# Kernel optimization log

Measured on AMD Instinct MI355X. Metric: run time of the kernel, lower is better.

The kernel has to match this reference:

```python
import jax, jax.numpy as jnp
import numpy as np

SIGMA = 1.0

def setup_inputs() -> dict:
    key = jax.random.key(0)
    k1, k2 = jax.random.split(key)
    N, IN, OUT = 524288, 64, 128
    x = jax.random.normal(k1, (N, IN), dtype=jnp.float32)
    bin_centers = jax.random.normal(k2, (OUT, IN), dtype=jnp.float32)
    return {"x": x, "bin_centers": bin_centers}

def reference(x, bin_centers):
    # distances[n,o] = sum_i (x[n,i] - c[o,i])^2 = ||x_n||^2 - 2 x_n.c_o + ||c_o||^2
    x2 = jnp.sum(x * x, axis=1)[:, None]                # [N,1]
    c2 = jnp.sum(bin_centers * bin_centers, axis=1)[None, :]  # [1,O]
    xc = jnp.einsum('ni,oi->no', x, bin_centers)        # [N,O] GEMM
    distances = x2 - 2.0 * xc + c2                      # [N,O]
    rbf = jnp.exp(-distances / (2.0 * SIGMA ** 2))      # [N,O]
    # histogram[o,i] = sum_n rbf[n,o] * x[n,i]  ->  rbf^T @ x
    histogram = jnp.einsum('no,ni->oi', rbf, x)         # [O,I] GEMM
    return histogram
```

## Files before the change

kernel.cpp:

```cpp
#include <hip/hip_runtime.h>
#include <stdint.h>


typedef __bf16 bf16x8 __attribute__((ext_vector_type(8)));
typedef unsigned short ushortx8 __attribute__((ext_vector_type(8)));
typedef float floatx4 __attribute__((ext_vector_type(4)));

#define GRIDN 1024
#define NSTRIPS 16384
#define LOG2E 1.4426950408889634f

#if __has_builtin(__builtin_amdgcn_exp2f)
#define EXP2F(x) __builtin_amdgcn_exp2f(x)
#else
#define EXP2F(x) exp2f(x)
#endif

static __device__ __forceinline__ unsigned int bfbits(float f) {
  unsigned int u = __float_as_uint(f);
  return u + 0x7fffu + ((u >> 16) & 1u);
}
static __device__ __forceinline__ unsigned int pkbf(float a, float b) {
  return (bfbits(a) >> 16) | (bfbits(b) & 0xffff0000u);
}

static __device__ __forceinline__ floatx4 mfma_bf16(ushortx8 a, ushortx8 b, floatx4 c) {
  return __builtin_amdgcn_mfma_f32_16x16x32_bf16(
      __builtin_bit_cast(bf16x8, a), __builtin_bit_cast(bf16x8, b), c, 0, 0, 0);
}

#define LSTR 72
#define PSTR 40

__global__ __launch_bounds__(128, 2) void rbf_hist_kernel(
    const float* __restrict__ x, const float* __restrict__ c,
    float* __restrict__ out, float* __restrict__ ws, int use_ws) {
  __shared__ unsigned short sXhi[32][LSTR];
  __shared__ unsigned short sXlo[32][LSTR];
  __shared__ unsigned short sXT [64][PSTR];
  __shared__ unsigned short sPw [2][64][PSTR];
  __shared__ float          sX2 [32];

  const int t    = threadIdx.x;
  const int lane = t & 63;
  const int w    = t >> 6;
  const int l15  = lane & 15;
  const int quad = lane >> 4;

  uint4 chi[4][2], clo[4][2];
  float m2c[4];
#pragma unroll
  for (int oo = 0; oo < 4; ++oo) {
    const int ot = 4 * w + oo;
    float sq = 0.f;
#pragma unroll
    for (int s = 0; s < 2; ++s) {
      const float* p = c + (ot * 16 + l15) * 64 + s * 32 + quad * 8;
      float4 va = *(const float4*)(p);
      float4 vb = *(const float4*)(p + 4);
      float f[8] = {va.x, va.y, va.z, va.w, vb.x, vb.y, vb.z, vb.w};
      unsigned int h[4], l[4];
#pragma unroll
      for (int jp = 0; jp < 4; ++jp) {
        float a = f[2 * jp], b = f[2 * jp + 1];
        sq = fmaf(a, a, sq);
        sq = fmaf(b, b, sq);
        a *= LOG2E; b *= LOG2E;
        unsigned int hp = pkbf(a, b);
        float la = a - __uint_as_float(hp << 16);
        float lb = b - __uint_as_float(hp & 0xffff0000u);
        h[jp] = hp;
        l[jp] = pkbf(la, lb);
      }
      chi[oo][s] = uint4{h[0], h[1], h[2], h[3]};
      clo[oo][s] = uint4{l[0], l[1], l[2], l[3]};
    }
    sq += __shfl_xor(sq, 16);
    sq += __shfl_xor(sq, 32);
    m2c[oo] = -0.5f * LOG2E * sq;
  }

  floatx4 hacc[4][4];
#pragma unroll
  for (int a = 0; a < 4; ++a)
#pragma unroll
    for (int b = 0; b < 4; ++b) {
      floatx4 z = {0.f, 0.f, 0.f, 0.f};
      hacc[a][b] = z;
    }

  const int r = t >> 2, q = t & 3;
  float4 v[4];
  {
    const size_t row0 = (size_t)(blockIdx.x * 32 + r) * 64;
#pragma unroll
    for (int g = 0; g < 4; ++g)
      v[g] = *(const float4*)(x + row0 + q * 4 + g * 16);
  }

  for (int it = 0; it < NSTRIPS / GRIDN; ++it) {
    __syncthreads();

    {
      float sq = 0.f;
#pragma unroll
      for (int g = 0; g < 4; ++g) {
        const int col = q * 4 + g * 16;
        float f0 = v[g].x, f1 = v[g].y, f2 = v[g].z, f3 = v[g].w;
        sq = fmaf(f0, f0, sq); sq = fmaf(f1, f1, sq);
        sq = fmaf(f2, f2, sq); sq = fmaf(f3, f3, sq);
        unsigned int h01 = pkbf(f0, f1), h23 = pkbf(f2, f3);
        float l0 = f0 - __uint_as_float(h01 << 16);
        float l1 = f1 - __uint_as_float(h01 & 0xffff0000u);
        float l2 = f2 - __uint_as_float(h23 << 16);
        float l3 = f3 - __uint_as_float(h23 & 0xffff0000u);
        uint2 hh = {h01, h23};
        uint2 ll = {pkbf(l0, l1), pkbf(l2, l3)};
        *(uint2*)&sXhi[r][col] = hh;
        *(uint2*)&sXlo[r][col] = ll;
        sXT[col + 0][r] = (unsigned short)(h01 & 0xffffu);
        sXT[col + 1][r] = (unsigned short)(h01 >> 16);
        sXT[col + 2][r] = (unsigned short)(h23 & 0xffffu);
        sXT[col + 3][r] = (unsigned short)(h23 >> 16);
      }
      sq += __shfl_xor(sq, 1);
      sq += __shfl_xor(sq, 2);
      if (q == 0) sX2[r] = -0.5f * LOG2E * sq;
    }
    __syncthreads();

    if (it < NSTRIPS / GRIDN - 1) {
      const size_t nrow = (size_t)((blockIdx.x + (it + 1) * GRIDN) * 32 + r) * 64;
#pragma unroll
      for (int g = 0; g < 4; ++g)
        v[g] = *(const float4*)(x + nrow + q * 4 + g * 16);
    }

#pragma unroll
    for (int t2 = 0; t2 < 2; ++t2) {
      ushortx8 xh0 = *(const ushortx8*)&sXhi[t2 * 16 + l15][quad * 8];
      ushortx8 xh1 = *(const ushortx8*)&sXhi[t2 * 16 + l15][32 + quad * 8];
      ushortx8 xl0 = *(const ushortx8*)&sXlo[t2 * 16 + l15][quad * 8];
      ushortx8 xl1 = *(const ushortx8*)&sXlo[t2 * 16 + l15][32 + quad * 8];
      float4 m2x = *(const float4*)&sX2[t2 * 16 + quad * 4];

#pragma unroll
      for (int oo = 0; oo < 4; ++oo) {
        floatx4 accA = {m2x.x + m2c[oo], m2x.y + m2c[oo],
                        m2x.z + m2c[oo], m2x.w + m2c[oo]};
        floatx4 accB = {0.f, 0.f, 0.f, 0.f};
        accA = mfma_bf16(xh0, __builtin_bit_cast(ushortx8, chi[oo][0]), accA);
        accB = mfma_bf16(xh1, __builtin_bit_cast(ushortx8, clo[oo][1]), accB);
        accA = mfma_bf16(xh1, __builtin_bit_cast(ushortx8, chi[oo][1]), accA);
        accB = mfma_bf16(xl0, __builtin_bit_cast(ushortx8, chi[oo][0]), accB);
        accA = mfma_bf16(xh0, __builtin_bit_cast(ushortx8, clo[oo][0]), accA);
        accB = mfma_bf16(xl1, __builtin_bit_cast(ushortx8, chi[oo][1]), accB);
        floatx4 acc = accA + accB;
        unsigned int r01 = pkbf(EXP2F(acc[0]), EXP2F(acc[1]));
        unsigned int r23 = pkbf(EXP2F(acc[2]), EXP2F(acc[3]));
        unsigned short* bp = &sPw[w][oo * 16 + l15][t2 * 16 + quad * 4];
        *(unsigned int*)(bp)     = r01;
        *(unsigned int*)(bp + 2) = r23;
      }
    }

    {
      ushortx8 a0 = *(const ushortx8*)&sPw[w][0 * 16 + l15][quad * 8];
      ushortx8 a1 = *(const ushortx8*)&sPw[w][1 * 16 + l15][quad * 8];
      ushortx8 a2 = *(const ushortx8*)&sPw[w][2 * 16 + l15][quad * 8];
      ushortx8 a3 = *(const ushortx8*)&sPw[w][3 * 16 + l15][quad * 8];
#pragma unroll
      for (int itl = 0; itl < 4; ++itl) {
        ushortx8 b = *(const ushortx8*)&sXT[itl * 16 + l15][quad * 8];
        hacc[0][itl] = mfma_bf16(a0, b, hacc[0][itl]);
        hacc[1][itl] = mfma_bf16(a1, b, hacc[1][itl]);
        hacc[2][itl] = mfma_bf16(a2, b, hacc[2][itl]);
        hacc[3][itl] = mfma_bf16(a3, b, hacc[3][itl]);
      }
    }
  }

  if (use_ws) {
    float* part = ws + (size_t)blockIdx.x * 8192;
#pragma unroll
    for (int oo = 0; oo < 4; ++oo)
#pragma unroll
      for (int itl = 0; itl < 4; ++itl)
#pragma unroll
        for (int e = 0; e < 4; ++e) {
          int o = (4 * w + oo) * 16 + quad * 4 + e;
          int i = itl * 16 + l15;
          part[o * 64 + i] = hacc[oo][itl][e];
        }
  } else {
#pragma unroll
    for (int oo = 0; oo < 4; ++oo)
#pragma unroll
      for (int itl = 0; itl < 4; ++itl)
#pragma unroll
        for (int e = 0; e < 4; ++e) {
          int o = (4 * w + oo) * 16 + quad * 4 + e;
          int i = itl * 16 + l15;
          atomicAdd(out + o * 64 + i, hacc[oo][itl][e]);
        }
  }
}

__global__ void reduce_kernel(const float* __restrict__ ws, float* __restrict__ out) {
  const int tid = blockIdx.x * 256 + threadIdx.x;
  const int e = tid & 8191;
  const int part = tid >> 13;
  const float* p = ws + (size_t)part * 256 * 8192 + e;
  float s = 0.f;
#pragma unroll 8
  for (int b = 0; b < 256; ++b) s += p[(size_t)b * 8192];
  atomicAdd(out + e, s);
}

__global__ void zero_out_kernel(float* out, int n) {
  int i = blockIdx.x * 256 + threadIdx.x;
  if (i < n) out[i] = 0.f;
}

extern "C" void kernel_launch(void* const* d_in, const int* in_sizes, int n_in,
                              void* d_out, int out_size, void* d_ws, size_t ws_size,
                              hipStream_t stream) {
  (void)in_sizes; (void)n_in;
  const float* x = (const float*)d_in[0];
  const float* c = (const float*)d_in[1];
  float* out = (float*)d_out;
  float* ws  = (float*)d_ws;

  const int use_ws = (ws_size >= (size_t)GRIDN * 8192 * sizeof(float)) ? 1 : 0;

  zero_out_kernel<<<(out_size + 255) / 256, 256, 0, stream>>>(out, out_size);
  rbf_hist_kernel<<<GRIDN, 128, 0, stream>>>(x, c, out, ws, use_ws);
  if (use_ws)
    reduce_kernel<<<128, 256, 0, stream>>>(ws, out);
}
```

Baseline: 214.4 us.

## Switch RBF histogram kernel from bf16 to fp16 MFMA with scaled exponent

Moves the distance GEMM from bf16 hi/lo splitting to fp16, which drops the x low-part term and cuts the distance MFMAs from six to four per tile. Exponentials get a +38 bias in log2 space so they fit fp16 range, and the final accumulators are multiplied by 2^-38 to undo it. The LDS round trips for the probability tile and the transposed x tile are removed. P now stays in registers as MFMA fragments, and the x transpose is done in registers by multiplying by an identity matrix with an extra MFMA. This trades shared-memory traffic and barriers for extra MFMA work, and risks fp16 overflow or underflow for extreme distances.

```diff
diff --git a/kernel.cpp b/kernel.cpp
--- a/kernel.cpp
+++ b/kernel.cpp
@@ -2,13 +2,16 @@
 #include <stdint.h>
 
 
-typedef __bf16 bf16x8 __attribute__((ext_vector_type(8)));
-typedef unsigned short ushortx8 __attribute__((ext_vector_type(8)));
+typedef _Float16 half8v __attribute__((ext_vector_type(8)));
+typedef _Float16 half4v __attribute__((ext_vector_type(4)));
+typedef __fp16  fp16x2 __attribute__((ext_vector_type(2)));
 typedef float floatx4 __attribute__((ext_vector_type(4)));
 
 #define GRIDN 1024
-#define NSTRIPS 16384
+#define NITER 16
 #define LOG2E 1.4426950408889634f
+#define PBIAS 38.0f
+#define PUNSCALE 3.637978807091713e-12f
 
 #if __has_builtin(__builtin_amdgcn_exp2f)
 #define EXP2F(x) __builtin_amdgcn_exp2f(x)
@@ -16,30 +19,39 @@
 #define EXP2F(x) exp2f(x)
 #endif
 
-static __device__ __forceinline__ unsigned int bfbits(float f) {
-  unsigned int u = __float_as_uint(f);
-  return u + 0x7fffu + ((u >> 16) & 1u);
-}
-static __device__ __forceinline__ unsigned int pkbf(float a, float b) {
-  return (bfbits(a) >> 16) | (bfbits(b) & 0xffff0000u);
-}
-
-static __device__ __forceinline__ floatx4 mfma_bf16(ushortx8 a, ushortx8 b, floatx4 c) {
-  return __builtin_amdgcn_mfma_f32_16x16x32_bf16(
-      __builtin_bit_cast(bf16x8, a), __builtin_bit_cast(bf16x8, b), c, 0, 0, 0);
+static __device__ __forceinline__ unsigned int pk16z(float a, float b) {
+  fp16x2 h = __builtin_amdgcn_cvt_pkrtz(a, b);
+  return __builtin_bit_cast(unsigned int, h);
+}
+static __device__ __forceinline__ unsigned int pk16(float a, float b) {
+  unsigned short ha = __builtin_bit_cast(unsigned short, (_Float16)a);
+  unsigned short hb = __builtin_bit_cast(unsigned short, (_Float16)b);
+  return (unsigned int)ha | ((unsigned int)hb << 16);
+}
+static __device__ __forceinline__ half4v mkh4(unsigned int lo, unsigned int hi) {
+  uint2 u{lo, hi};
+  return __builtin_bit_cast(half4v, u);
+}
+static __device__ __forceinline__ half8v mkh8(unsigned int a, unsigned int b,
+                                              unsigned int c, unsigned int d) {
+  uint4 u{a, b, c, d};
+  return __builtin_bit_cast(half8v, u);
+}
+
+static __device__ __forceinline__ floatx4 mfma32(half8v a, half8v b, floatx4 c) {
+  return __builtin_amdgcn_mfma_f32_16x16x32_f16(a, b, c, 0, 0, 0);
+}
+static __device__ __forceinline__ floatx4 mfma16(half4v a, half4v b, floatx4 c) {
+  return __builtin_amdgcn_mfma_f32_16x16x16f16(a, b, c, 0, 0, 0);
 }
 
 #define LSTR 72
-#define PSTR 40
 
 __global__ __launch_bounds__(128, 2) void rbf_hist_kernel(
     const float* __restrict__ x, const float* __restrict__ c,
     float* __restrict__ out, float* __restrict__ ws, int use_ws) {
-  __shared__ unsigned short sXhi[32][LSTR];
-  __shared__ unsigned short sXlo[32][LSTR];
-  __shared__ unsigned short sXT [64][PSTR];
-  __shared__ unsigned short sPw [2][64][PSTR];
-  __shared__ float          sX2 [32];
+  __shared__ unsigned short sXh[32][LSTR];
+  __shared__ float          sX2[32];
 
   const int t    = threadIdx.x;
   const int lane = t & 63;
@@ -47,7 +59,7 @@
   const int l15  = lane & 15;
   const int quad = lane >> 4;
 
-  uint4 chi[4][2], clo[4][2];
+  half8v chi[4][2], clo[4][2];
   float m2c[4];
 #pragma unroll
   for (int oo = 0; oo < 4; ++oo) {
@@ -66,18 +78,27 @@
         sq = fmaf(a, a, sq);
         sq = fmaf(b, b, sq);
         a *= LOG2E; b *= LOG2E;
-        unsigned int hp = pkbf(a, b);
-        float la = a - __uint_as_float(hp << 16);
-        float lb = b - __uint_as_float(hp & 0xffff0000u);
+        unsigned int hp = pk16(a, b);
+        float ha = (float)__builtin_bit_cast(_Float16, (unsigned short)(hp & 0xffffu));
+        float hb = (float)__builtin_bit_cast(_Float16, (unsigned short)(hp >> 16));
         h[jp] = hp;
-        l[jp] = pkbf(la, lb);
-      }
-      chi[oo][s] = uint4{h[0], h[1], h[2], h[3]};
-      clo[oo][s] = uint4{l[0], l[1], l[2], l[3]};
+        l[jp] = pk16z(a - ha, b - hb);
+      }
+      chi[oo][s] = mkh8(h[0], h[1], h[2], h[3]);
+      clo[oo][s] = mkh8(l[0], l[1], l[2], l[3]);
     }
     sq += __shfl_xor(sq, 16);
     sq += __shfl_xor(sq, 32);
-    m2c[oo] = -0.5f * LOG2E * sq;
+    m2c[oo] = fmaf(-0.5f * LOG2E, sq, PBIAS);
+  }
+
+  half4v iden;
+  {
+    float e0 = (quad * 4 + 0 == l15) ? 1.f : 0.f;
+    float e1 = (quad * 4 + 1 == l15) ? 1.f : 0.f;
+    float e2 = (quad * 4 + 2 == l15) ? 1.f : 0.f;
+    float e3 = (quad * 4 + 3 == l15) ? 1.f : 0.f;
+    iden = mkh4(pk16z(e0, e1), pk16z(e2, e3));
   }
 
   floatx4 hacc[4][4];
@@ -92,92 +113,81 @@
   const int r = t >> 2, q = t & 3;
   float4 v[4];
   {
-    const size_t row0 = (size_t)(blockIdx.x * 32 + r) * 64;
-#pragma unroll
-    for (int g = 0; g < 4; ++g)
-      v[g] = *(const float4*)(x + row0 + q * 4 + g * 16);
-  }
-
-  for (int it = 0; it < NSTRIPS / GRIDN; ++it) {
+    const size_t row0 = (size_t)(blockIdx.x * 32 + r) * 64 + q * 16;
+#pragma unroll
+    for (int u = 0; u < 4; ++u)
+      v[u] = *(const float4*)(x + row0 + u * 4);
+  }
+
+  for (int it = 0; it < NITER; ++it) {
     __syncthreads();
 
     {
       float sq = 0.f;
-#pragma unroll
-      for (int g = 0; g < 4; ++g) {
-        const int col = q * 4 + g * 16;
-        float f0 = v[g].x, f1 = v[g].y, f2 = v[g].z, f3 = v[g].w;
+      unsigned int hw[8];
+#pragma unroll
+      for (int u = 0; u < 4; ++u) {
+        float f0 = v[u].x, f1 = v[u].y, f2 = v[u].z, f3 = v[u].w;
         sq = fmaf(f0, f0, sq); sq = fmaf(f1, f1, sq);
         sq = fmaf(f2, f2, sq); sq = fmaf(f3, f3, sq);
-        unsigned int h01 = pkbf(f0, f1), h23 = pkbf(f2, f3);
-        float l0 = f0 - __uint_as_float(h01 << 16);
-        float l1 = f1 - __uint_as_float(h01 & 0xffff0000u);
-        float l2 = f2 - __uint_as_float(h23 << 16);
-        float l3 = f3 - __uint_as_float(h23 & 0xffff0000u);
-        uint2 hh = {h01, h23};
-        uint2 ll = {pkbf(l0, l1), pkbf(l2, l3)};
-        *(uint2*)&sXhi[r][col] = hh;
-        *(uint2*)&sXlo[r][col] = ll;
-        sXT[col + 0][r] = (unsigned short)(h01 & 0xffffu);
-        sXT[col + 1][r] = (unsigned short)(h01 >> 16);
-        sXT[col + 2][r] = (unsigned short)(h23 & 0xffffu);
-        sXT[col + 3][r] = (unsigned short)(h23 >> 16);
-      }
+        hw[2 * u]     = pk16(f0, f1);
+        hw[2 * u + 1] = pk16(f2, f3);
+      }
+      *(uint4*)&sXh[r][q * 16]     = uint4{hw[0], hw[1], hw[2], hw[3]};
+      *(uint4*)&sXh[r][q * 16 + 8] = uint4{hw[4], hw[5], hw[6], hw[7]};
       sq += __shfl_xor(sq, 1);
       sq += __shfl_xor(sq, 2);
       if (q == 0) sX2[r] = -0.5f * LOG2E * sq;
     }
     __syncthreads();
 
-    if (it < NSTRIPS / GRIDN - 1) {
-      const size_t nrow = (size_t)((blockIdx.x + (it + 1) * GRIDN) * 32 + r) * 64;
-#pragma unroll
-      for (int g = 0; g < 4; ++g)
-        v[g] = *(const float4*)(x + nrow + q * 4 + g * 16);
-    }
-
+    if (it < NITER - 1) {
+      const size_t nrow =
+          (size_t)((blockIdx.x + (it + 1) * GRIDN) * 32 + r) * 64 + q * 16;
+#pragma unroll
+      for (int u = 0; u < 4; ++u)
+        v[u] = *(const float4*)(x + nrow + u * 4);
+    }
+
+    half4v P[4][2];
 #pragma unroll
     for (int t2 = 0; t2 < 2; ++t2) {
-      ushortx8 xh0 = *(const ushortx8*)&sXhi[t2 * 16 + l15][quad * 8];
-      ushortx8 xh1 = *(const ushortx8*)&sXhi[t2 * 16 + l15][32 + quad * 8];
-      ushortx8 xl0 = *(const ushortx8*)&sXlo[t2 * 16 + l15][quad * 8];
-      ushortx8 xl1 = *(const ushortx8*)&sXlo[t2 * 16 + l15][32 + quad * 8];
+      half8v xh0 = *(const half8v*)&sXh[t2 * 16 + l15][quad * 8];
+      half8v xh1 = *(const half8v*)&sXh[t2 * 16 + l15][32 + quad * 8];
       float4 m2x = *(const float4*)&sX2[t2 * 16 + quad * 4];
-
 #pragma unroll
       for (int oo = 0; oo < 4; ++oo) {
         floatx4 accA = {m2x.x + m2c[oo], m2x.y + m2c[oo],
                         m2x.z + m2c[oo], m2x.w + m2c[oo]};
         floatx4 accB = {0.f, 0.f, 0.f, 0.f};
-        accA = mfma_bf16(xh0, __builtin_bit_cast(ushortx8, chi[oo][0]), accA);
-        accB = mfma_bf16(xh1, __builtin_bit_cast(ushortx8, clo[oo][1]), accB);
-        accA = mfma_bf16(xh1, __builtin_bit_cast(ushortx8, chi[oo][1]), accA);
-        accB = mfma_bf16(xl0, __builtin_bit_cast(ushortx8, chi[oo][0]), accB);
-        accA = mfma_bf16(xh0, __builtin_bit_cast(ushortx8, clo[oo][0]), accA);
-        accB = mfma_bf16(xl1, __builtin_bit_cast(ushortx8, chi[oo][1]), accB);
+        accA = mfma32(xh0, chi[oo][0], accA);
+        accB = mfma32(xh1, clo[oo][1], accB);
+        accA = mfma32(xh1, chi[oo][1], accA);
+        accB = mfma32(xh0, clo[oo][0], accB);
         floatx4 acc = accA + accB;
-        unsigned int r01 = pkbf(EXP2F(acc[0]), EXP2F(acc[1]));
-        unsigned int r23 = pkbf(EXP2F(acc[2]), EXP2F(acc[3]));
-        unsigned short* bp = &sPw[w][oo * 16 + l15][t2 * 16 + quad * 4];
-        *(unsigned int*)(bp)     = r01;
-        *(unsigned int*)(bp + 2) = r23;
-      }
-    }
-
-    {
-      ushortx8 a0 = *(const ushortx8*)&sPw[w][0 * 16 + l15][quad * 8];
-      ushortx8 a1 = *(const ushortx8*)&sPw[w][1 * 16 + l15][quad * 8];
-      ushortx8 a2 = *(const ushortx8*)&sPw[w][2 * 16 + l15][quad * 8];
-      ushortx8 a3 = *(const ushortx8*)&sPw[w][3 * 16 + l15][quad * 8];
+        P[oo][t2] = mkh4(pk16(EXP2F(acc[0]), EXP2F(acc[1])),
+                         pk16(EXP2F(acc[2]), EXP2F(acc[3])));
+      }
+    }
+
+    half4v XT[4][2];
+#pragma unroll
+    for (int t2 = 0; t2 < 2; ++t2)
 #pragma unroll
       for (int itl = 0; itl < 4; ++itl) {
-        ushortx8 b = *(const ushortx8*)&sXT[itl * 16 + l15][quad * 8];
-        hacc[0][itl] = mfma_bf16(a0, b, hacc[0][itl]);
-        hacc[1][itl] = mfma_bf16(a1, b, hacc[1][itl]);
-        hacc[2][itl] = mfma_bf16(a2, b, hacc[2][itl]);
-        hacc[3][itl] = mfma_bf16(a3, b, hacc[3][itl]);
-      }
-    }
+        half4v ax = *(const half4v*)&sXh[t2 * 16 + l15][itl * 16 + quad * 4];
+        floatx4 z = {0.f, 0.f, 0.f, 0.f};
+        floatx4 d = mfma16(ax, iden, z);
+        XT[itl][t2] = mkh4(pk16z(d[0], d[1]), pk16z(d[2], d[3]));
+      }
+
+#pragma unroll
+    for (int t2 = 0; t2 < 2; ++t2)
+#pragma unroll
+      for (int oo = 0; oo < 4; ++oo)
+#pragma unroll
+        for (int itl = 0; itl < 4; ++itl)
+          hacc[oo][itl] = mfma16(P[oo][t2], XT[itl][t2], hacc[oo][itl]);
   }
 
   if (use_ws) {
@@ -190,7 +200,7 @@
         for (int e = 0; e < 4; ++e) {
           int o = (4 * w + oo) * 16 + quad * 4 + e;
           int i = itl * 16 + l15;
-          part[o * 64 + i] = hacc[oo][itl][e];
+          part[o * 64 + i] = hacc[oo][itl][e] * PUNSCALE;
         }
   } else {
 #pragma unroll
@@ -201,7 +211,7 @@
         for (int e = 0; e < 4; ++e) {
           int o = (4 * w + oo) * 16 + quad * 4 + e;
           int i = itl * 16 + l15;
-          atomicAdd(out + o * 64 + i, hacc[oo][itl][e]);
+          atomicAdd(out + o * 64 + i, hacc[oo][itl][e] * PUNSCALE);
         }
   }
 }
```

After: 207.3 us. -3.3%, faster.
